# Kernel tuning notes

Measured on AMD Instinct MI355X. Metric: run time of the kernel, lower is better.

The kernel has to match this reference:

```python
import jax, jax.numpy as jnp
import numpy as np

B, S, H, NH = 4, 2048, 512, 8  # batch, seq, hidden, heads
D = H // NH                    # head dim = 64


def setup_inputs() -> dict:
    key = jax.random.key(0)
    ks = jax.random.split(key, 12)
    wscale = 1.0 / np.sqrt(H)
    mk = lambda k, sh: jax.random.normal(k, sh, jnp.float32)
    return {
        "q": mk(ks[0], (B, S, H)),
        "k": mk(ks[1], (B, S, H)),
        "v": mk(ks[2], (B, S, H)),
        "k_b": mk(ks[3], (B, S, H)),
        "mask": jax.random.randint(ks[4], (B, S), 0, 2).astype(jnp.int32),
        "Wq": mk(ks[5], (H, H)) * wscale, "bq": jnp.zeros((H,), jnp.float32),
        "Wk": mk(ks[6], (H, H)) * wscale, "bk": jnp.zeros((H,), jnp.float32),
        "Wv": mk(ks[7], (H, H)) * wscale, "bv": jnp.zeros((H,), jnp.float32),
        "Wkb": mk(ks[8], (H, H)) * wscale, "bkb": jnp.zeros((H,), jnp.float32),
        "Wo": mk(ks[9], (H, H)) * wscale, "bo": jnp.zeros((H,), jnp.float32),
    }


def _attn(q, k, v, k_b, mask, Wq, bq, Wk, bk, Wv, bv, Wkb, bkb, Wo, bo):
    b, s, h = q.shape
    proj = lambda x, W, bias: (x @ W + bias).reshape(b, s, NH, D).transpose(0, 2, 1, 3)
    qh = proj(q, Wq, bq)      # [b, nh, s, d]
    kh = proj(k, Wk, bk)
    vh = proj(v, Wv, bv)
    kbh = proj(k_b, Wkb, bkb)
    # q@k^T + q@k_b^T == q@(k+k_b)^T, scaled by sqrt(d)
    corr = jnp.einsum('bhqd,bhkd->bhqk', qh, kh + kbh) / jnp.sqrt(jnp.float32(D))
    # torch mask repeat pattern depends only on key index -> broadcast over q and heads
    corr = jnp.where(mask[:, None, None, :] == 0, jnp.float32(-1e9), corr)
    prob = jax.nn.softmax(corr, axis=-1)  # dropout inactive (eval mode)
    hid = jnp.einsum('bhqk,bhkd->bhqd', prob, vh)
    hid = hid.transpose(0, 2, 1, 3).reshape(b, s, h)
    return hid @ Wo + bo


def reference(q, k, v, k_b, mask, Wq, bq, Wk, bk, Wv, bv, Wkb, bkb, Wo, bo):
    return _attn(q, k, v, k_b, mask, Wq, bq, Wk, bk, Wv, bv, Wkb, bkb, Wo, bo)
```

## Files before the change

kernel.cpp:

```cpp
#include <hip/hip_runtime.h>
#include <hip/hip_bf16.h>
#include <math.h>

#define B_  4
#define S_  2048
#define H_  512
#define NH_ 8
#define D_  64

typedef __attribute__((ext_vector_type(8))) short bf16x8;
typedef __attribute__((ext_vector_type(4))) float f32x4;
typedef __attribute__((ext_vector_type(16))) float f32x16;
#define MFMA16(a, b, c) __builtin_amdgcn_mfma_f32_16x16x32_bf16(a, b, c, 0, 0, 0)
#define MFMA32(a, b, c) __builtin_amdgcn_mfma_f32_32x32x16_bf16(a, b, c, 0, 0, 0)

__device__ __forceinline__ unsigned short f2bf(float f) {
    union { float f; unsigned int i; } x; x.f = f;
    unsigned int i = x.i;
    i += 0x7fffu + ((i >> 16) & 1u);
    return (unsigned short)(i >> 16);
}
__device__ __forceinline__ unsigned int pk2(float lo, float hi) {
    union { __hip_bfloat162 h; unsigned int u; } c;
    c.h = __float22bfloat162_rn(make_float2(lo, hi));
    return c.u;
}
__device__ __forceinline__ void gl_lds16(const void* g, void* l) {
    __builtin_amdgcn_global_load_lds(
        (const __attribute__((address_space(1))) unsigned int*)g,
        (__attribute__((address_space(3))) unsigned int*)l, 16, 0, 0);
}

__global__ __launch_bounds__(256) void prep_w(
    const float* __restrict__ W0, const float* __restrict__ W1,
    const float* __restrict__ W2, const float* __restrict__ W3,
    unsigned short* __restrict__ Wt)
{
    const float* Ws[4] = {W0, W1, W2, W3};
    const float* W = Ws[blockIdx.z];
    unsigned short* Y = Wt + (size_t)blockIdx.z * H_ * H_;
    __shared__ float Tl[64][68];
    const int t = threadIdx.x;
    const int k0 = blockIdx.y * 64, n0 = blockIdx.x * 64;
    #pragma unroll
    for (int i = 0; i < 4; ++i) {
        const int e = (t + 256 * i) * 4;
        const int r = e >> 6, c = e & 63;
        const float4 a = *(const float4*)(W + (size_t)(k0 + r) * H_ + n0 + c);
        Tl[c + 0][r] = a.x; Tl[c + 1][r] = a.y;
        Tl[c + 2][r] = a.z; Tl[c + 3][r] = a.w;
    }
    __syncthreads();
    #pragma unroll
    for (int i = 0; i < 4; ++i) {
        const int e = (t + 256 * i) * 4;
        const int n = e >> 6, c = e & 63;
        uint2 p;
        p.x = pk2(Tl[n][c + 0], Tl[n][c + 1]);
        p.y = pk2(Tl[n][c + 2], Tl[n][c + 3]);
        *(uint2*)(Y + (size_t)(n0 + n) * H_ + k0 + c) = p;
    }
}

__global__ __launch_bounds__(256, 3) void proj_all(
    const float* __restrict__ q,  const float* __restrict__ k,
    const float* __restrict__ v,  const float* __restrict__ k_b,
    const unsigned short* __restrict__ Wt,
    const float* __restrict__ bq, const float* __restrict__ bk,
    const float* __restrict__ bkb,const float* __restrict__ bv,
    unsigned short* __restrict__ Qf, unsigned short* __restrict__ Kf,
    unsigned short* __restrict__ Vf)
{
    __shared__ __align__(16) unsigned short LB[17408];
    unsigned short* As = LB;
    unsigned short* Bs = LB + 8192;

    const int z = blockIdx.z;
    const float *X, *bias, *X2 = nullptr, *bias2 = nullptr;
    const unsigned short *Wa, *Wb = nullptr;
    unsigned short* Y;
    bool VT = false;
    const size_t WSZ = (size_t)H_ * H_;
    if (z == 0)      { X = q; Wa = Wt;           bias = bq; Y = Qf; }
    else if (z == 1) { X = k; Wa = Wt + WSZ;     bias = bk;
                       X2 = k_b; Wb = Wt + 2 * WSZ; bias2 = bkb; Y = Kf; }
    else             { X = v; Wa = Wt + 3 * WSZ; bias = bv; Y = Vf; VT = true; }

    const int t = threadIdx.x;
    const int w = t >> 6, lane = t & 63;
    const int quad = lane >> 4, l15 = lane & 15;
    const int wr = w >> 1, wc = w & 1;
    const int m0 = blockIdx.x * 128, n0 = blockIdx.y * 128;

    const f32x4 zero = {0.f, 0.f, 0.f, 0.f};
    f32x4 acc[4][4];
    #pragma unroll
    for (int i = 0; i < 4; ++i)
        #pragma unroll
        for (int j = 0; j < 4; ++j) acc[i][j] = zero;

    const int npass = (X2 != nullptr) ? 2 : 1;
    for (int pass = 0; pass < npass; ++pass) {
        const float* Xp = pass ? X2 : X;
        const unsigned short* Wp = pass ? Wb : Wa;
        for (int kb0 = 0; kb0 < H_; kb0 += 64) {
            __syncthreads();
            #pragma unroll
            for (int i = 0; i < 4; ++i) {
                const int c = w * 4 + i;
                const int u = c * 64 + lane;
                const int row = u >> 3;
                const int sc  = ((u & 7) ^ (row & 7)) << 3;
                gl_lds16(Wp + (size_t)(n0 + row) * H_ + kb0 + sc, Bs + c * 512);
            }
            float4 av[8];
            #pragma unroll
            for (int i = 0; i < 8; ++i) {
                const int e = (t + 256 * i) * 4;
                av[i] = *(const float4*)(Xp + (size_t)(m0 + (e >> 6)) * H_ + kb0 + (e & 63));
            }
            #pragma unroll
            for (int i = 0; i < 8; ++i) {
                const int e = (t + 256 * i) * 4;
                const int row = e >> 6, kc = e & 63;
                uint2 p; p.x = pk2(av[i].x, av[i].y); p.y = pk2(av[i].z, av[i].w);
                *(uint2*)&As[row * 64 + ((((kc >> 3) ^ (row & 7)) << 3) | (kc & 7))] = p;
            }
            __syncthreads();
            #pragma unroll
            for (int ks = 0; ks < 2; ++ks) {
                bf16x8 af[4], bfr[4];
                #pragma unroll
                for (int i = 0; i < 4; ++i) {
                    const int row = wr * 64 + i * 16 + l15;
                    af[i] = *(const bf16x8*)&As[row * 64 +
                                (((ks * 4 + quad) ^ (row & 7)) << 3)];
                }
                #pragma unroll
                for (int j = 0; j < 4; ++j) {
                    const int nrw = wc * 64 + j * 16 + l15;
                    bfr[j] = *(const bf16x8*)&Bs[nrw * 64 +
                                (((ks * 4 + quad) ^ (nrw & 7)) << 3)];
                }
                #pragma unroll
                for (int i = 0; i < 4; ++i)
                    #pragma unroll
                    for (int j = 0; j < 4; ++j)
                        acc[i][j] = MFMA16(af[i], bfr[j], acc[i][j]);
            }
        }
    }

    const int bb = m0 >> 11, s0 = m0 & (S_ - 1);
    if (!VT) {
        #pragma unroll
        for (int i = 0; i < 4; ++i)
            #pragma unroll
            for (int r = 0; r < 4; ++r) {
                const int s = s0 + wr * 64 + i * 16 + quad * 4 + r;
                #pragma unroll
                for (int j = 0; j < 4; ++j) {
                    const int nn = n0 + wc * 64 + j * 16 + l15;
                    const int h = nn >> 6, d = nn & 63;
                    float val = acc[i][j][r] + bias[nn];
                    if (bias2) val += bias2[nn];
                    Y[(((size_t)bb * NH_ + h) * S_ + s) * D_ + d] = f2bf(val);
                }
            }
    } else {
        __syncthreads();
        #pragma unroll
        for (int i = 0; i < 4; ++i)
            #pragma unroll
            for (int r = 0; r < 4; ++r) {
                const int ml = wr * 64 + i * 16 + quad * 4 + r;
                #pragma unroll
                for (int j = 0; j < 4; ++j) {
                    const int nl = wc * 64 + j * 16 + l15;
                    LB[nl * 136 + ml] = f2bf(acc[i][j][r] + bias[n0 + nl]);
                }
            }
        __syncthreads();
        const int nr = t >> 1, half = t & 1;
        const int nn = n0 + nr, h = nn >> 6, d = nn & 63;
        const size_t vbase = (((size_t)bb * NH_ + h) * D_ + d) * S_ + s0 + half * 64;
        #pragma unroll
        for (int i = 0; i < 16; ++i)
            *(ushort4*)(Y + vbase + i * 4) =
                *(const ushort4*)&LB[nr * 136 + half * 64 + i * 4];
    }
}

__global__ __launch_bounds__(256) void attn_mfma(
    unsigned short* QHd,
    const unsigned short* __restrict__ Kh, const unsigned short* __restrict__ Vt,
    const int* __restrict__ mask)
{
    const int b = blockIdx.z, h = blockIdx.y;
    const int q0 = blockIdx.x * 128;
    const int t = threadIdx.x;
    const int w = t >> 6, lane = t & 63;
    const int hi = lane >> 5, l31 = lane & 31;

    __shared__ __align__(16) unsigned short KsL[2 * 4096];
    __shared__ __align__(16) unsigned short VsL[2 * 4096];
    __shared__ float mskf[S_];

    const size_t head = ((size_t)b * NH_ + h) * S_;
    unsigned short* Qbase = QHd + head * D_;
    const unsigned short* Kbase = Kh + head * D_;
    const unsigned short* Vbase = Vt + head * D_;

    for (int i = t; i < S_; i += 256)
        mskf[i] = (mask[b * S_ + i] == 0) ? -1e9f : 0.f;

    bf16x8 qf[4];
    #pragma unroll
    for (int ks = 0; ks < 4; ++ks)
        qf[ks] = *(const bf16x8*)(
            Qbase + (size_t)(q0 + w * 32 + l31) * D_ + ks * 16 + hi * 8);

    f32x16 O0, O1;
    #pragma unroll
    for (int i = 0; i < 16; ++i) { O0[i] = 0.f; O1[i] = 0.f; }
    float lsum = 0.f;
    const float SC2 = 0.125f * 1.44269504089f;

    #define STAGE(kt_) do {                                                        \
        const int bf_ = (kt_) & 1, k0_ = (kt_) * 64;                               \
        _Pragma("unroll")                                                          \
        for (int i_ = 0; i_ < 2; ++i_) {                                           \
            const int c_ = w * 2 + i_;                                             \
            const int u_ = c_ * 64 + lane;                                         \
            const int row_ = u_ >> 3;                                              \
            const int sc_ = ((u_ & 7) ^ (row_ & 7)) << 3;                          \
            gl_lds16(Kbase + (size_t)(k0_ + row_) * D_ + sc_,                      \
                     KsL + bf_ * 4096 + c_ * 512);                                 \
            gl_lds16(Vbase + (size_t)row_ * S_ + k0_ + sc_,                        \
                     VsL + bf_ * 4096 + c_ * 512);                                 \
        }                                                                          \
    } while (0)

    STAGE(0);
    __syncthreads();

    for (int kt = 0; kt < S_ / 64; ++kt) {
        const int bf = kt & 1;
        const int k0 = kt * 64;
        if (kt + 1 < S_ / 64) STAGE(kt + 1);

        bf16x8 pfrag[4];
        #pragma unroll
        for (int kb = 0; kb < 2; ++kb) {
            f32x16 acc;
            #pragma unroll
            for (int i = 0; i < 16; ++i) acc[i] = 0.f;
            const int krow = kb * 32 + l31;
            const unsigned short* Kb = KsL + bf * 4096 + krow * 64;
            const int rwk = krow & 7;
            __builtin_amdgcn_s_setprio(1);
            #pragma unroll
            for (int ks = 0; ks < 4; ++ks) {
                const bf16x8 kf = *(const bf16x8*)&Kb[(((ks * 2 + hi) ^ rwk) << 3)];
                acc = MFMA32(kf, qf[ks], acc);
            }
            __builtin_amdgcn_s_setprio(0);
            float p[16];
            #pragma unroll
            for (int bq = 0; bq < 4; ++bq) {
                const float4 ms4 = *(const float4*)&mskf[k0 + kb * 32 + bq * 8 + hi * 4];
                p[4 * bq + 0] = __builtin_amdgcn_exp2f(fmaf(acc[4 * bq + 0], SC2, ms4.x));
                p[4 * bq + 1] = __builtin_amdgcn_exp2f(fmaf(acc[4 * bq + 1], SC2, ms4.y));
                p[4 * bq + 2] = __builtin_amdgcn_exp2f(fmaf(acc[4 * bq + 2], SC2, ms4.z));
                p[4 * bq + 3] = __builtin_amdgcn_exp2f(fmaf(acc[4 * bq + 3], SC2, ms4.w));
            }
            lsum += ((p[0] + p[1]) + (p[2] + p[3])) + ((p[4] + p[5]) + (p[6] + p[7]))
                  + ((p[8] + p[9]) + (p[10] + p[11])) + ((p[12] + p[13]) + (p[14] + p[15]));
            unsigned pkv[8];
            #pragma unroll
            for (int bq = 0; bq < 4; ++bq) {
                pkv[2 * bq + 0] = pk2(p[4 * bq + 0], p[4 * bq + 1]);
                pkv[2 * bq + 1] = pk2(p[4 * bq + 2], p[4 * bq + 3]);
            }
            #pragma unroll
            for (int ksl = 0; ksl < 2; ++ksl) {
                unsigned m0 = pkv[4 * ksl + 0], m2 = pkv[4 * ksl + 2];
                asm volatile("v_permlane32_swap_b32 %0, %1" : "+v"(m0), "+v"(m2));
                unsigned m1 = pkv[4 * ksl + 1], m3 = pkv[4 * ksl + 3];
                asm volatile("v_permlane32_swap_b32 %0, %1" : "+v"(m1), "+v"(m3));
                union { unsigned u[4]; bf16x8 v; } pu;
                pu.u[0] = m0; pu.u[1] = m1; pu.u[2] = m2; pu.u[3] = m3;
                pfrag[kb * 2 + ksl] = pu.v;
            }
        }
        __builtin_amdgcn_s_setprio(1);
        #pragma unroll
        for (int dblk = 0; dblk < 2; ++dblk) {
            const int vrow = dblk * 32 + l31;
            const unsigned short* Vb = VsL + bf * 4096 + vrow * 64;
            const int rwv = vrow & 7;
            #pragma unroll
            for (int ks = 0; ks < 4; ++ks) {
                const bf16x8 vf = *(const bf16x8*)&Vb[(((ks * 2 + hi) ^ rwv) << 3)];
                if (dblk == 0) O0 = MFMA32(vf, pfrag[ks], O0);
                else           O1 = MFMA32(vf, pfrag[ks], O1);
            }
        }
        __builtin_amdgcn_s_setprio(0);
        __syncthreads();
    }
    #undef STAGE

    lsum += __shfl_xor(lsum, 32, 64);
    const float inv = 1.f / lsum;

    unsigned short* Orow = Qbase + (size_t)(q0 + w * 32 + l31) * D_;
    #pragma unroll
    for (int dblk = 0; dblk < 2; ++dblk) {
        #pragma unroll
        for (int bq = 0; bq < 4; ++bq) {
            const float v0 = (dblk ? O1[4 * bq + 0] : O0[4 * bq + 0]) * inv;
            const float v1 = (dblk ? O1[4 * bq + 1] : O0[4 * bq + 1]) * inv;
            const float v2 = (dblk ? O1[4 * bq + 2] : O0[4 * bq + 2]) * inv;
            const float v3 = (dblk ? O1[4 * bq + 3] : O0[4 * bq + 3]) * inv;
            uint2 st; st.x = pk2(v0, v1); st.y = pk2(v2, v3);
            *(uint2*)&Orow[dblk * 32 + bq * 8 + hi * 4] = st;
        }
    }
}

__global__ __launch_bounds__(256) void out_mfma(
    const unsigned short* __restrict__ Hd, const unsigned short* __restrict__ Wot,
    const float* __restrict__ bias, float* __restrict__ Out)
{
    __shared__ __align__(16) unsigned short As[8192];
    __shared__ __align__(16) unsigned short Bs[4096];
    const int t = threadIdx.x;
    const int w = t >> 6, lane = t & 63;
    const int quad = lane >> 4, l15 = lane & 15;
    const int wr = w >> 1, wc = w & 1;
    const int m0 = blockIdx.x * 128, n0 = blockIdx.y * 64;
    const int bb = m0 >> 11, s0 = m0 & (S_ - 1);

    const f32x4 zero = {0.f, 0.f, 0.f, 0.f};
    f32x4 acc[4][2];
    #pragma unroll
    for (int i = 0; i < 4; ++i)
        #pragma unroll
        for (int j = 0; j < 2; ++j) acc[i][j] = zero;

    for (int kb0 = 0; kb0 < H_; kb0 += 64) {
        const int hk = kb0 >> 6;
        const unsigned short* Ab = Hd + (((size_t)bb * NH_ + hk) * S_ + s0) * D_;
        __syncthreads();
        #pragma unroll
        for (int i = 0; i < 4; ++i) {
            const int c = w * 4 + i, u = c * 64 + lane, row = u >> 3;
            const int sc = ((u & 7) ^ (row & 7)) << 3;
            gl_lds16(Ab + (size_t)row * D_ + sc, As + c * 512);
        }
        #pragma unroll
        for (int i = 0; i < 2; ++i) {
            const int c = w * 2 + i, u = c * 64 + lane, row = u >> 3;
            const int sc = ((u & 7) ^ (row & 7)) << 3;
            gl_lds16(Wot + (size_t)(n0 + row) * H_ + kb0 + sc, Bs + c * 512);
        }
        __syncthreads();
        #pragma unroll
        for (int ks = 0; ks < 2; ++ks) {
            bf16x8 af[4], bfr[2];
            #pragma unroll
            for (int i = 0; i < 4; ++i) {
                const int row = wr * 64 + i * 16 + l15;
                af[i] = *(const bf16x8*)&As[row * 64 +
                            (((ks * 4 + quad) ^ (row & 7)) << 3)];
            }
            #pragma unroll
            for (int j = 0; j < 2; ++j) {
                const int nrw = wc * 32 + j * 16 + l15;
                bfr[j] = *(const bf16x8*)&Bs[nrw * 64 +
                            (((ks * 4 + quad) ^ (nrw & 7)) << 3)];
            }
            #pragma unroll
            for (int i = 0; i < 4; ++i)
                #pragma unroll
                for (int j = 0; j < 2; ++j)
                    acc[i][j] = MFMA16(af[i], bfr[j], acc[i][j]);
        }
    }
    #pragma unroll
    for (int i = 0; i < 4; ++i)
        #pragma unroll
        for (int r = 0; r < 4; ++r) {
            const int m = m0 + wr * 64 + i * 16 + quad * 4 + r;
            #pragma unroll
            for (int j = 0; j < 2; ++j) {
                const int n = n0 + wc * 32 + j * 16 + l15;
                Out[(size_t)m * H_ + n] = acc[i][j][r] + bias[n];
            }
        }
}

__global__ void fill_kernel(float* __restrict__ out, float val, int n) {
    const int i = blockIdx.x * 256 + threadIdx.x;
    if (i < n) out[i] = val;
}

extern "C" void kernel_launch(void* const* d_in, const int* in_sizes, int n_in,
                              void* d_out, int out_size, void* d_ws, size_t ws_size,
                              hipStream_t stream) {
    const float* q   = (const float*)d_in[0];
    const float* k   = (const float*)d_in[1];
    const float* v   = (const float*)d_in[2];
    const float* k_b = (const float*)d_in[3];
    const int*   msk = (const int*)d_in[4];
    const float* Wq  = (const float*)d_in[5];
    const float* bq  = (const float*)d_in[6];
    const float* Wk  = (const float*)d_in[7];
    const float* bk  = (const float*)d_in[8];
    const float* Wv  = (const float*)d_in[9];
    const float* bv  = (const float*)d_in[10];
    const float* Wkb = (const float*)d_in[11];
    const float* bkb = (const float*)d_in[12];
    const float* Wo  = (const float*)d_in[13];
    const float* bo  = (const float*)d_in[14];
    float* out = (float*)d_out;

    const size_t PER  = (size_t)B_ * NH_ * S_ * D_;
    const size_t NEED = 3 * PER * sizeof(unsigned short);
    if (ws_size < NEED) {
        fill_kernel<<<(out_size + 255) / 256, 256, 0, stream>>>(
            out, (float)((ws_size >> 20) + 2), out_size);
        return;
    }
    unsigned short* wsh = (unsigned short*)d_ws;
    unsigned short* Qf  = wsh;
    unsigned short* Kf  = wsh + PER;
    unsigned short* Vf  = wsh + 2 * PER;

    unsigned short* Wt = (unsigned short*)d_out;

    dim3 gw(8, 8, 4);
    prep_w<<<gw, 256, 0, stream>>>(Wq, Wk, Wkb, Wv, Wt);

    dim3 gp((B_ * S_) / 128, H_ / 128, 3);
    proj_all<<<gp, 256, 0, stream>>>(q, k, v, k_b, Wt, bq, bk, bkb, bv, Qf, Kf, Vf);

    dim3 ga(S_ / 128, NH_, B_);
    attn_mfma<<<ga, 256, 0, stream>>>(Qf, Kf, Vf, msk);

    dim3 gw1(8, 8, 1);
    prep_w<<<gw1, 256, 0, stream>>>(Wo, Wo, Wo, Wo, Kf);

    dim3 go((B_ * S_) / 128, H_ / 64, 1);
    out_mfma<<<go, 256, 0, stream>>>(Qf, Kf, bo, out);
}
```

Before: 232.8 us.

## Double-buffer LDS tiles in projection and output GEMM kernels

Both the fused QKV projection kernel and the output projection kernel now use two LDS buffers. The loads for the next k-step (async global-to-LDS copies for weights and Hd, plus register prefetch of fp32 activations) are issued before the MFMA work on the current buffer, and each step needs only one barrier. The aim is to hide global memory latency behind matrix math. In exchange the projection kernel's LDS use doubles and its launch-bounds occupancy hint drops from 3 to 2 blocks, which may reduce latency hiding across blocks.

Measured after the change: 244.8 us. +5.2%, slower.

```diff
diff --git a/kernel.cpp b/kernel.cpp
--- a/kernel.cpp
+++ b/kernel.cpp
@@ -62,7 +62,7 @@
     }
 }
 
-__global__ __launch_bounds__(256, 3) void proj_all(
+__global__ __launch_bounds__(256, 2) void proj_all(
     const float* __restrict__ q,  const float* __restrict__ k,
     const float* __restrict__ v,  const float* __restrict__ k_b,
     const unsigned short* __restrict__ Wt,
@@ -71,9 +71,7 @@
     unsigned short* __restrict__ Qf, unsigned short* __restrict__ Kf,
     unsigned short* __restrict__ Vf)
 {
-    __shared__ __align__(16) unsigned short LB[17408];
-    unsigned short* As = LB;
-    unsigned short* Bs = LB + 8192;
+    __shared__ __align__(16) unsigned short LB[32768];
 
     const int z = blockIdx.z;
     const float *X, *bias, *X2 = nullptr, *bias2 = nullptr;
@@ -99,57 +97,87 @@
         #pragma unroll
         for (int j = 0; j < 4; ++j) acc[i][j] = zero;
 
-    const int npass = (X2 != nullptr) ? 2 : 1;
-    for (int pass = 0; pass < npass; ++pass) {
-        const float* Xp = pass ? X2 : X;
-        const unsigned short* Wp = pass ? Wb : Wa;
-        for (int kb0 = 0; kb0 < H_; kb0 += 64) {
-            __syncthreads();
+    const int NS = (X2 != nullptr) ? 16 : 8;
+
+    #define STAGE_B(s_, bfx_) do {                                             \
+        const unsigned short* Wp_ = ((s_) >> 3) ? Wb : Wa;                     \
+        const int kb0_ = ((s_) & 7) * 64;                                      \
+        unsigned short* Bd_ = LB + (bfx_) * 16384 + 8192;                      \
+        _Pragma("unroll")                                                      \
+        for (int i_ = 0; i_ < 4; ++i_) {                                       \
+            const int c_ = w * 4 + i_;                                         \
+            const int u_ = c_ * 64 + lane;                                     \
+            const int row_ = u_ >> 3;                                          \
+            const int sc_ = ((u_ & 7) ^ (row_ & 7)) << 3;                      \
+            gl_lds16(Wp_ + (size_t)(n0 + row_) * H_ + kb0_ + sc_,              \
+                     Bd_ + c_ * 512);                                          \
+        }                                                                      \
+    } while (0)
+
+    #define LOAD_A(av_, s_) do {                                               \
+        const float* Xp_ = ((s_) >> 3) ? X2 : X;                               \
+        const int kb0_ = ((s_) & 7) * 64;                                      \
+        _Pragma("unroll")                                                      \
+        for (int i_ = 0; i_ < 8; ++i_) {                                       \
+            const int e_ = (t + 256 * i_) * 4;                                 \
+            av_[i_] = *(const float4*)(Xp_ + (size_t)(m0 + (e_ >> 6)) * H_     \
+                                       + kb0_ + (e_ & 63));                    \
+        }                                                                      \
+    } while (0)
+
+    #define CVT_WRITE_A(av_, bfx_) do {                                        \
+        unsigned short* Ad_ = LB + (bfx_) * 16384;                             \
+        _Pragma("unroll")                                                      \
+        for (int i_ = 0; i_ < 8; ++i_) {                                       \
+            const int e_ = (t + 256 * i_) * 4;                                 \
+            const int row_ = e_ >> 6, kc_ = e_ & 63;                           \
+            uint2 p_; p_.x = pk2(av_[i_].x, av_[i_].y);                        \
+            p_.y = pk2(av_[i_].z, av_[i_].w);                                  \
+            *(uint2*)&Ad_[row_ * 64 +                                          \
+                ((((kc_ >> 3) ^ (row_ & 7)) << 3) | (kc_ & 7))] = p_;          \
+        }                                                                      \
+    } while (0)
+
+    float4 av[8];
+    STAGE_B(0, 0);
+    LOAD_A(av, 0);
+    CVT_WRITE_A(av, 0);
+    __syncthreads();
+
+    for (int s = 0; s < NS; ++s) {
+        const int cur = s & 1, nxt = cur ^ 1;
+        const bool more = (s + 1 < NS);
+        if (more) { STAGE_B(s + 1, nxt); LOAD_A(av, s + 1); }
+
+        const unsigned short* Ac = LB + cur * 16384;
+        const unsigned short* Bc = LB + cur * 16384 + 8192;
+        #pragma unroll
+        for (int ks = 0; ks < 2; ++ks) {
+            bf16x8 af[4], bfr[4];
             #pragma unroll
             for (int i = 0; i < 4; ++i) {
-                const int c = w * 4 + i;
-                const int u = c * 64 + lane;
-                const int row = u >> 3;
-                const int sc  = ((u & 7) ^ (row & 7)) << 3;
-                gl_lds16(Wp + (size_t)(n0 + row) * H_ + kb0 + sc, Bs + c * 512);
-            }
-            float4 av[8];
-            #pragma unroll
-            for (int i = 0; i < 8; ++i) {
-                const int e = (t + 256 * i) * 4;
-                av[i] = *(const float4*)(Xp + (size_t)(m0 + (e >> 6)) * H_ + kb0 + (e & 63));
-            }
-            #pragma unroll
-            for (int i = 0; i < 8; ++i) {
-                const int e = (t + 256 * i) * 4;
-                const int row = e >> 6, kc = e & 63;
-                uint2 p; p.x = pk2(av[i].x, av[i].y); p.y = pk2(av[i].z, av[i].w);
-                *(uint2*)&As[row * 64 + ((((kc >> 3) ^ (row & 7)) << 3) | (kc & 7))] = p;
-            }
-            __syncthreads();
-            #pragma unroll
-            for (int ks = 0; ks < 2; ++ks) {
-                bf16x8 af[4], bfr[4];
+                const int row = wr * 64 + i * 16 + l15;
+                af[i] = *(const bf16x8*)&Ac[row * 64 +
+                            (((ks * 4 + quad) ^ (row & 7)) << 3)];
+            }
+            #pragma unroll
+            for (int j = 0; j < 4; ++j) {
+                const int nrw = wc * 64 + j * 16 + l15;
+                bfr[j] = *(const bf16x8*)&Bc[nrw * 64 +
+                            (((ks * 4 + quad) ^ (nrw & 7)) << 3)];
+            }
+            #pragma unroll
+            for (int i = 0; i < 4; ++i)
                 #pragma unroll
-                for (int i = 0; i < 4; ++i) {
-                    const int row = wr * 64 + i * 16 + l15;
-                    af[i] = *(const bf16x8*)&As[row * 64 +
-                                (((ks * 4 + quad) ^ (row & 7)) << 3)];
-                }
-                #pragma unroll
-                for (int j = 0; j < 4; ++j) {
-                    const int nrw = wc * 64 + j * 16 + l15;
-                    bfr[j] = *(const bf16x8*)&Bs[nrw * 64 +
-                                (((ks * 4 + quad) ^ (nrw & 7)) << 3)];
-                }
-                #pragma unroll
-                for (int i = 0; i < 4; ++i)
-                    #pragma unroll
-                    for (int j = 0; j < 4; ++j)
-                        acc[i][j] = MFMA16(af[i], bfr[j], acc[i][j]);
-            }
-        }
-    }
+                for (int j = 0; j < 4; ++j)
+                    acc[i][j] = MFMA16(af[i], bfr[j], acc[i][j]);
+        }
+        if (more) CVT_WRITE_A(av, nxt);
+        __syncthreads();
+    }
+    #undef STAGE_B
+    #undef LOAD_A
+    #undef CVT_WRITE_A
 
     const int bb = m0 >> 11, s0 = m0 & (S_ - 1);
     if (!VT) {
@@ -333,8 +361,8 @@
     const unsigned short* __restrict__ Hd, const unsigned short* __restrict__ Wot,
     const float* __restrict__ bias, float* __restrict__ Out)
 {
-    __shared__ __align__(16) unsigned short As[8192];
-    __shared__ __align__(16) unsigned short Bs[4096];
+    __shared__ __align__(16) unsigned short As2[2][8192];
+    __shared__ __align__(16) unsigned short Bs2[2][4096];
     const int t = threadIdx.x;
     const int w = t >> 6, lane = t & 63;
     const int quad = lane >> 4, l15 = lane & 15;
@@ -349,36 +377,44 @@
         #pragma unroll
         for (int j = 0; j < 2; ++j) acc[i][j] = zero;
 
-    for (int kb0 = 0; kb0 < H_; kb0 += 64) {
-        const int hk = kb0 >> 6;
-        const unsigned short* Ab = Hd + (((size_t)bb * NH_ + hk) * S_ + s0) * D_;
-        __syncthreads();
-        #pragma unroll
-        for (int i = 0; i < 4; ++i) {
-            const int c = w * 4 + i, u = c * 64 + lane, row = u >> 3;
-            const int sc = ((u & 7) ^ (row & 7)) << 3;
-            gl_lds16(Ab + (size_t)row * D_ + sc, As + c * 512);
-        }
-        #pragma unroll
-        for (int i = 0; i < 2; ++i) {
-            const int c = w * 2 + i, u = c * 64 + lane, row = u >> 3;
-            const int sc = ((u & 7) ^ (row & 7)) << 3;
-            gl_lds16(Wot + (size_t)(n0 + row) * H_ + kb0 + sc, Bs + c * 512);
-        }
-        __syncthreads();
+    #define OSTAGE(s_, bfx_) do {                                              \
+        const int hk_ = (s_);                                                  \
+        const unsigned short* Ab_ = Hd + (((size_t)bb * NH_ + hk_) * S_ + s0)  \
+                                    * D_;                                      \
+        _Pragma("unroll")                                                      \
+        for (int i_ = 0; i_ < 4; ++i_) {                                       \
+            const int c_ = w * 4 + i_, u_ = c_ * 64 + lane, row_ = u_ >> 3;    \
+            const int sc_ = ((u_ & 7) ^ (row_ & 7)) << 3;                      \
+            gl_lds16(Ab_ + (size_t)row_ * D_ + sc_, As2[bfx_] + c_ * 512);     \
+        }                                                                      \
+        _Pragma("unroll")                                                      \
+        for (int i_ = 0; i_ < 2; ++i_) {                                       \
+            const int c_ = w * 2 + i_, u_ = c_ * 64 + lane, row_ = u_ >> 3;    \
+            const int sc_ = ((u_ & 7) ^ (row_ & 7)) << 3;                      \
+            gl_lds16(Wot + (size_t)(n0 + row_) * H_ + hk_ * 64 + sc_,          \
+                     Bs2[bfx_] + c_ * 512);                                    \
+        }                                                                      \
+    } while (0)
+
+    OSTAGE(0, 0);
+    __syncthreads();
+
+    for (int s = 0; s < 8; ++s) {
+        const int cur = s & 1;
+        if (s + 1 < 8) OSTAGE(s + 1, cur ^ 1);
         #pragma unroll
         for (int ks = 0; ks < 2; ++ks) {
             bf16x8 af[4], bfr[2];
             #pragma unroll
             for (int i = 0; i < 4; ++i) {
                 const int row = wr * 64 + i * 16 + l15;
-                af[i] = *(const bf16x8*)&As[row * 64 +
+                af[i] = *(const bf16x8*)&As2[cur][row * 64 +
                             (((ks * 4 + quad) ^ (row & 7)) << 3)];
             }
             #pragma unroll
             for (int j = 0; j < 2; ++j) {
                 const int nrw = wc * 32 + j * 16 + l15;
-                bfr[j] = *(const bf16x8*)&Bs[nrw * 64 +
+                bfr[j] = *(const bf16x8*)&Bs2[cur][nrw * 64 +
                             (((ks * 4 + quad) ^ (nrw & 7)) << 3)];
             }
             #pragma unroll
@@ -387,7 +423,10 @@
                 for (int j = 0; j < 2; ++j)
                     acc[i][j] = MFMA16(af[i], bfr[j], acc[i][j]);
         }
-    }
+        __syncthreads();
+    }
+    #undef OSTAGE
+
     #pragma unroll
     for (int i = 0; i < 4; ++i)
         #pragma unroll
```

## Split key tile across waves and halve query block to raise occupancy

Applied to the files above, without the earlier changes.

Each attention block now covers 64 queries instead of 128, with its four waves arranged as two query groups times two key halves of each 64-key tile. Partial output accumulators and row sums from the second key half are reduced through LDS before normalization and store. The grid doubles and launch bounds request four blocks per CU, aiming for better latency hiding and load balance. In exchange, K/V tiles are loaded twice as often overall and an extra LDS reduction is added.

New measurement: 232.1 us. No clear change (-0.3%).

```diff
diff --git a/kernel.cpp b/kernel.cpp
--- a/kernel.cpp
+++ b/kernel.cpp
@@ -191,16 +191,17 @@
     }
 }
 
-__global__ __launch_bounds__(256) void attn_mfma(
+__global__ __launch_bounds__(256, 4) void attn_mfma(
     unsigned short* QHd,
     const unsigned short* __restrict__ Kh, const unsigned short* __restrict__ Vt,
     const int* __restrict__ mask)
 {
     const int b = blockIdx.z, h = blockIdx.y;
-    const int q0 = blockIdx.x * 128;
+    const int q0 = blockIdx.x * 64;
     const int t = threadIdx.x;
     const int w = t >> 6, lane = t & 63;
     const int hi = lane >> 5, l31 = lane & 31;
+    const int qg = w & 1, kh = w >> 1;
 
     __shared__ __align__(16) unsigned short KsL[2 * 4096];
     __shared__ __align__(16) unsigned short VsL[2 * 4096];
@@ -218,7 +219,7 @@
     #pragma unroll
     for (int ks = 0; ks < 4; ++ks)
         qf[ks] = *(const bf16x8*)(
-            Qbase + (size_t)(q0 + w * 32 + l31) * D_ + ks * 16 + hi * 8);
+            Qbase + (size_t)(q0 + qg * 32 + l31) * D_ + ks * 16 + hi * 8);
 
     f32x16 O0, O1;
     #pragma unroll
@@ -249,49 +250,46 @@
         const int k0 = kt * 64;
         if (kt + 1 < S_ / 64) STAGE(kt + 1);
 
-        bf16x8 pfrag[4];
-        #pragma unroll
-        for (int kb = 0; kb < 2; ++kb) {
-            f32x16 acc;
-            #pragma unroll
-            for (int i = 0; i < 16; ++i) acc[i] = 0.f;
-            const int krow = kb * 32 + l31;
-            const unsigned short* Kb = KsL + bf * 4096 + krow * 64;
-            const int rwk = krow & 7;
-            __builtin_amdgcn_s_setprio(1);
-            #pragma unroll
-            for (int ks = 0; ks < 4; ++ks) {
-                const bf16x8 kf = *(const bf16x8*)&Kb[(((ks * 2 + hi) ^ rwk) << 3)];
-                acc = MFMA32(kf, qf[ks], acc);
-            }
-            __builtin_amdgcn_s_setprio(0);
-            float p[16];
-            #pragma unroll
-            for (int bq = 0; bq < 4; ++bq) {
-                const float4 ms4 = *(const float4*)&mskf[k0 + kb * 32 + bq * 8 + hi * 4];
-                p[4 * bq + 0] = __builtin_amdgcn_exp2f(fmaf(acc[4 * bq + 0], SC2, ms4.x));
-                p[4 * bq + 1] = __builtin_amdgcn_exp2f(fmaf(acc[4 * bq + 1], SC2, ms4.y));
-                p[4 * bq + 2] = __builtin_amdgcn_exp2f(fmaf(acc[4 * bq + 2], SC2, ms4.z));
-                p[4 * bq + 3] = __builtin_amdgcn_exp2f(fmaf(acc[4 * bq + 3], SC2, ms4.w));
-            }
-            lsum += ((p[0] + p[1]) + (p[2] + p[3])) + ((p[4] + p[5]) + (p[6] + p[7]))
-                  + ((p[8] + p[9]) + (p[10] + p[11])) + ((p[12] + p[13]) + (p[14] + p[15]));
-            unsigned pkv[8];
-            #pragma unroll
-            for (int bq = 0; bq < 4; ++bq) {
-                pkv[2 * bq + 0] = pk2(p[4 * bq + 0], p[4 * bq + 1]);
-                pkv[2 * bq + 1] = pk2(p[4 * bq + 2], p[4 * bq + 3]);
-            }
-            #pragma unroll
-            for (int ksl = 0; ksl < 2; ++ksl) {
-                unsigned m0 = pkv[4 * ksl + 0], m2 = pkv[4 * ksl + 2];
-                asm volatile("v_permlane32_swap_b32 %0, %1" : "+v"(m0), "+v"(m2));
-                unsigned m1 = pkv[4 * ksl + 1], m3 = pkv[4 * ksl + 3];
-                asm volatile("v_permlane32_swap_b32 %0, %1" : "+v"(m1), "+v"(m3));
-                union { unsigned u[4]; bf16x8 v; } pu;
-                pu.u[0] = m0; pu.u[1] = m1; pu.u[2] = m2; pu.u[3] = m3;
-                pfrag[kb * 2 + ksl] = pu.v;
-            }
+        f32x16 acc;
+        #pragma unroll
+        for (int i = 0; i < 16; ++i) acc[i] = 0.f;
+        const int krow = kh * 32 + l31;
+        const unsigned short* Kb = KsL + bf * 4096 + krow * 64;
+        const int rwk = krow & 7;
+        __builtin_amdgcn_s_setprio(1);
+        #pragma unroll
+        for (int ks = 0; ks < 4; ++ks) {
+            const bf16x8 kf = *(const bf16x8*)&Kb[(((ks * 2 + hi) ^ rwk) << 3)];
+            acc = MFMA32(kf, qf[ks], acc);
+        }
+        __builtin_amdgcn_s_setprio(0);
+        float p[16];
+        #pragma unroll
+        for (int bq = 0; bq < 4; ++bq) {
+            const float4 ms4 = *(const float4*)&mskf[k0 + kh * 32 + bq * 8 + hi * 4];
+            p[4 * bq + 0] = __builtin_amdgcn_exp2f(fmaf(acc[4 * bq + 0], SC2, ms4.x));
+            p[4 * bq + 1] = __builtin_amdgcn_exp2f(fmaf(acc[4 * bq + 1], SC2, ms4.y));
+            p[4 * bq + 2] = __builtin_amdgcn_exp2f(fmaf(acc[4 * bq + 2], SC2, ms4.z));
+            p[4 * bq + 3] = __builtin_amdgcn_exp2f(fmaf(acc[4 * bq + 3], SC2, ms4.w));
+        }
+        lsum += ((p[0] + p[1]) + (p[2] + p[3])) + ((p[4] + p[5]) + (p[6] + p[7]))
+              + ((p[8] + p[9]) + (p[10] + p[11])) + ((p[12] + p[13]) + (p[14] + p[15]));
+        unsigned pkv[8];
+        #pragma unroll
+        for (int bq = 0; bq < 4; ++bq) {
+            pkv[2 * bq + 0] = pk2(p[4 * bq + 0], p[4 * bq + 1]);
+            pkv[2 * bq + 1] = pk2(p[4 * bq + 2], p[4 * bq + 3]);
+        }
+        bf16x8 pfrag[2];
+        #pragma unroll
+        for (int ksl = 0; ksl < 2; ++ksl) {
+            unsigned m0 = pkv[4 * ksl + 0], m2 = pkv[4 * ksl + 2];
+            asm volatile("v_permlane32_swap_b32 %0, %1" : "+v"(m0), "+v"(m2));
+            unsigned m1 = pkv[4 * ksl + 1], m3 = pkv[4 * ksl + 3];
+            asm volatile("v_permlane32_swap_b32 %0, %1" : "+v"(m1), "+v"(m3));
+            union { unsigned u[4]; bf16x8 v; } pu;
+            pu.u[0] = m0; pu.u[1] = m1; pu.u[2] = m2; pu.u[3] = m3;
+            pfrag[ksl] = pu.v;
         }
         __builtin_amdgcn_s_setprio(1);
         #pragma unroll
@@ -300,10 +298,11 @@
             const unsigned short* Vb = VsL + bf * 4096 + vrow * 64;
             const int rwv = vrow & 7;
             #pragma unroll
-            for (int ks = 0; ks < 4; ++ks) {
-                const bf16x8 vf = *(const bf16x8*)&Vb[(((ks * 2 + hi) ^ rwv) << 3)];
-                if (dblk == 0) O0 = MFMA32(vf, pfrag[ks], O0);
-                else           O1 = MFMA32(vf, pfrag[ks], O1);
+            for (int ksl = 0; ksl < 2; ++ksl) {
+                const bf16x8 vf =
+                    *(const bf16x8*)&Vb[(((kh * 4 + ksl * 2 + hi) ^ rwv) << 3)];
+                if (dblk == 0) O0 = MFMA32(vf, pfrag[ksl], O0);
+                else           O1 = MFMA32(vf, pfrag[ksl], O1);
             }
         }
         __builtin_amdgcn_s_setprio(0);
@@ -312,19 +311,37 @@
     #undef STAGE
 
     lsum += __shfl_xor(lsum, 32, 64);
-    const float inv = 1.f / lsum;
-
-    unsigned short* Orow = Qbase + (size_t)(q0 + w * 32 + l31) * D_;
-    #pragma unroll
-    for (int dblk = 0; dblk < 2; ++dblk) {
-        #pragma unroll
-        for (int bq = 0; bq < 4; ++bq) {
-            const float v0 = (dblk ? O1[4 * bq + 0] : O0[4 * bq + 0]) * inv;
-            const float v1 = (dblk ? O1[4 * bq + 1] : O0[4 * bq + 1]) * inv;
-            const float v2 = (dblk ? O1[4 * bq + 2] : O0[4 * bq + 2]) * inv;
-            const float v3 = (dblk ? O1[4 * bq + 3] : O0[4 * bq + 3]) * inv;
-            uint2 st; st.x = pk2(v0, v1); st.y = pk2(v2, v3);
-            *(uint2*)&Orow[dblk * 32 + bq * 8 + hi * 4] = st;
+
+    if (kh == 1) {
+        float* R = qg ? (float*)VsL : (float*)KsL;
+        #pragma unroll
+        for (int i = 0; i < 16; ++i) R[lane * 33 + i]      = O0[i];
+        #pragma unroll
+        for (int i = 0; i < 16; ++i) R[lane * 33 + 16 + i] = O1[i];
+        if (hi == 0) R[2112 + l31] = lsum;
+    }
+    __syncthreads();
+    if (kh == 0) {
+        const float* R = qg ? (const float*)VsL : (const float*)KsL;
+        #pragma unroll
+        for (int i = 0; i < 16; ++i) O0[i] += R[lane * 33 + i];
+        #pragma unroll
+        for (int i = 0; i < 16; ++i) O1[i] += R[lane * 33 + 16 + i];
+        lsum += R[2112 + l31];
+        const float inv = 1.f / lsum;
+
+        unsigned short* Orow = Qbase + (size_t)(q0 + qg * 32 + l31) * D_;
+        #pragma unroll
+        for (int dblk = 0; dblk < 2; ++dblk) {
+            #pragma unroll
+            for (int bq = 0; bq < 4; ++bq) {
+                const float v0 = (dblk ? O1[4 * bq + 0] : O0[4 * bq + 0]) * inv;
+                const float v1 = (dblk ? O1[4 * bq + 1] : O0[4 * bq + 1]) * inv;
+                const float v2 = (dblk ? O1[4 * bq + 2] : O0[4 * bq + 2]) * inv;
+                const float v3 = (dblk ? O1[4 * bq + 3] : O0[4 * bq + 3]) * inv;
+                uint2 st; st.x = pk2(v0, v1); st.y = pk2(v2, v3);
+                *(uint2*)&Orow[dblk * 32 + bq * 8 + hi * 4] = st;
+            }
         }
     }
 }
@@ -446,7 +463,7 @@
     dim3 gp((B_ * S_) / 128, H_ / 128, 3);
     proj_all<<<gp, 256, 0, stream>>>(q, k, v, k_b, Wt, bq, bk, bkb, bv, Qf, Kf, Vf);
 
-    dim3 ga(S_ / 128, NH_, B_);
+    dim3 ga(S_ / 64, NH_, B_);
     attn_mfma<<<ga, 256, 0, stream>>>(Qf, Kf, Vf, msk);
 
     dim3 gw1(8, 8, 1);
```
